# Kernel optimization log

Hardware: AMD Instinct MI355X
Metric: run time of the kernel (lower is better)

Reference implementation:

```python
import jax, jax.numpy as jnp
from jax import lax
import numpy as np

AXIS = 16      # axis_neuron
N_TYPES = 2    # number of atom types


def _mlp(x, Ws, bs):
    for W, b in zip(Ws, bs):
        x = jnp.tanh(x @ W + b)
    return x


def _forward(sym, dx, dy, dz, types,
             fw0, fb0, fw1, fb1, fw2, fb2,
             gw0, gb0, gw1, gb1, gw2, gb2, gwo, gbo):
    # sym/dx/dy/dz: (B, N, SEL, 4); types: (B, N) int
    N, SEL = sym.shape[1], sym.shape[2]

    def frame_fn(R, DX, DY, DZ, ty):
        E_atoms = jnp.zeros((N,), R.dtype)
        F = jnp.zeros((N, 3), R.dtype)
        for t in range(N_TYPES):  # loop over small fixed set of atom types
            mask = (ty == t).astype(R.dtype)            # (N,)
            cnt = jnp.maximum(mask.sum(), 1.0)
            m3 = mask[:, None, None]
            sji = R[:, :, 0:1]
            xyz = R[:, :, 1:4]
            ns = cnt * SEL
            nx = ns * 3.0
            s_avg = (sji * m3).sum() / ns
            x_avg = (xyz * m3).sum() / nx
            s_avg2 = ((sji ** 2) * m3).sum() / ns
            x_avg2 = ((xyz ** 2) * m3).sum() / nx
            avg2 = jnp.stack([s_avg2, x_avg2, x_avg2, x_avg2])
            avg1 = jnp.stack([s_avg, x_avg, x_avg, x_avg])
            std = jnp.sqrt(jnp.maximum(avg2 - avg1 ** 2, 0.0)) + 1e-8
            avg = jnp.stack([s_avg, 0.0 * s_avg, 0.0 * s_avg, 0.0 * s_avg])
            avg = lax.stop_gradient(avg)   # torch computes stats under no_grad
            std = lax.stop_gradient(std)
            Rn = (R - avg) / std
            DXn = DX / std
            DYn = DY / std
            DZn = DZ / std

            def etot(Rn_):
                s = Rn_[:, :, 0:1]                                  # (N, SEL, 1)
                G = _mlp(s, [fw0[t], fw1[t], fw2[t]], [fb0[t], fb1[t], fb2[t]])  # (N, SEL, M)
                RG = jnp.einsum('nsf,nsm->nfm', Rn_, G)             # (N, 4, M)
                GRRG = jnp.einsum('nfm,nfa->nma', RG, RG[:, :, :AXIS]).reshape(N, -1)  # (N, M*AXIS)
                denom = cnt * GRRG.shape[1]
                mu = (GRRG * mask[:, None]).sum() / denom
                mu2 = ((GRRG ** 2) * mask[:, None]).sum() / denom
                sd = jnp.sqrt(jnp.maximum(mu2 - mu ** 2, 0.0)) + 1e-8
                h = _mlp((GRRG - mu) / sd,
                         [gw0[t], gw1[t], gw2[t]], [gb0[t], gb1[t], gb2[t]])
                e = (h @ gwo[t] + gbo[t])[:, 0]                     # (N,)
                return (e * mask).sum(), e

            (Et, e_atoms), dR = jax.value_and_grad(etot, has_aux=True)(Rn)
            E_atoms = E_atoms + e_atoms * mask
            Fx = (dR * DXn).sum(axis=(1, 2))
            Fy = (dR * DYn).sum(axis=(1, 2))
            Fz = (dR * DZn).sum(axis=(1, 2))
            # "DO NOT forget to multiply -1 for F!!!"
            F = F - jnp.stack([Fx, Fy, Fz], axis=1) * mask[:, None]
        return E_atoms.sum(), F

    return jax.vmap(frame_fn)(sym, dx, dy, dz, types)


def setup_inputs() -> dict:
    key = jax.random.key(0)
    ks = jax.random.split(key, 24)
    B, N, SEL = 4, 1024, 128
    M = 100                     # filter_neuron[-1]
    FIT_IN = AXIS * M           # 1600
    d = {}
    d['sym'] = jax.random.normal(ks[0], (B, N, SEL, 4), jnp.float32)
    d['dx'] = jax.random.normal(ks[1], (B, N, SEL, 4), jnp.float32)
    d['dy'] = jax.random.normal(ks[2], (B, N, SEL, 4), jnp.float32)
    d['dz'] = jax.random.normal(ks[3], (B, N, SEL, 4), jnp.float32)
    d['types'] = jax.random.randint(ks[4], (B, N), 0, N_TYPES, jnp.int32)

    def w(k, shape):
        return jax.random.normal(k, shape, jnp.float32) / np.float32(np.sqrt(shape[-2]))

    def b(k, shape):
        return 0.1 * jax.random.normal(k, shape, jnp.float32)

    d['fw0'] = w(ks[5], (N_TYPES, 1, 25));      d['fb0'] = b(ks[6], (N_TYPES, 25))
    d['fw1'] = w(ks[7], (N_TYPES, 25, 50));     d['fb1'] = b(ks[8], (N_TYPES, 50))
    d['fw2'] = w(ks[9], (N_TYPES, 50, M));      d['fb2'] = b(ks[10], (N_TYPES, M))
    d['gw0'] = w(ks[11], (N_TYPES, FIT_IN, 240)); d['gb0'] = b(ks[12], (N_TYPES, 240))
    d['gw1'] = w(ks[13], (N_TYPES, 240, 240));  d['gb1'] = b(ks[14], (N_TYPES, 240))
    d['gw2'] = w(ks[15], (N_TYPES, 240, 240));  d['gb2'] = b(ks[16], (N_TYPES, 240))
    d['gwo'] = w(ks[17], (N_TYPES, 240, 1));    d['gbo'] = b(ks[18], (N_TYPES, 1))
    return d


def reference(sym, dx, dy, dz, types,
              fw0, fb0, fw1, fb1, fw2, fb2,
              gw0, gb0, gw1, gb1, gw2, gb2, gwo, gbo):
    return _forward(sym, dx, dy, dz, types,
                    fw0, fb0, fw1, fb1, fw2, fb2,
                    gw0, gb0, gw1, gb1, gw2, gb2, gwo, gbo)
```

## Files before the change

kernel.cpp:

```cpp
#include <hip/hip_runtime.h>

#define NBATCH 4
#define NATOM 1024
#define NSEL 128
#define H1 25
#define H2 50
#define HM 100
#define AX 16
#define GF 1600
#define FI 240
#define NT 2
#define NGRP64 18

#define WS_STATS_RAW 0
#define WS_STATS_FIN 64
#define WS_MUSD_RAW 128
#define WS_MUSD_FIN 144
#define WS_S_RAW 176
#define WS_CTR 192
#define WS_EBUF 256
#define WS_IDX (WS_EBUF + NBATCH*NATOM)
#define WS_G (WS_IDX + NBATCH*1152)
#define WS_P (WS_G + (size_t)NBATCH*NATOM*GF)
#define WS_BP0  (WS_P + (size_t)NBATCH*NATOM*GF)
#define WS_BP1  (WS_BP0 + (size_t)NT*15*50*256)
#define WS_BP2  (WS_BP1 + (size_t)NT*15*8*256)
#define WS_BPT2 (WS_BP2 + (size_t)NT*15*8*256)
#define WS_BPT1 (WS_BPT2 + (size_t)NT*15*8*256)
#define WS_BPT0 (WS_BPT1 + (size_t)NT*15*8*256)
#define WS_FW1T (WS_BPT0 + (size_t)NT*100*8*256)
#define WS_FW2T (WS_FW1T + (size_t)NT*H2*H1)
#define WS_RGB (WS_FW2T + (size_t)NT*HM*H2)
#define WS_GTB (WS_RGB + (size_t)NBATCH*NATOM*HM*4)
#define WS_GTB_UNITS ((size_t)NBATCH*NATOM*(HM/2)*NSEL)
#define WS_BF1B  (WS_GTB + WS_GTB_UNITS)
#define WS_BW2TB (WS_BF1B + (size_t)NT*1024)
#define WS_BW1TB (WS_BW2TB + (size_t)NT*4096)
#define WS_BF2B  (WS_BW1TB + (size_t)NT*1024)
#define WS_END   (WS_BF2B + (size_t)NT*3584)

#define GSTR 108

typedef __attribute__((ext_vector_type(8))) short bf16x8;
typedef __attribute__((ext_vector_type(4))) float f32x4;

__device__ __forceinline__ float ftanh(float x){
  float e = __expf(2.0f*x);
  return 1.0f - 2.0f/(e+1.0f);
}
__device__ __forceinline__ unsigned short f2bf(float x){
  unsigned b=__float_as_uint(x); b += 0x7FFF + ((b>>16)&1); return (unsigned short)(b>>16);
}
__device__ __forceinline__ float bf2f(unsigned short h){ return __uint_as_float(((unsigned)h)<<16); }
__device__ __forceinline__ float bflo(unsigned u){ return __uint_as_float(u<<16); }
__device__ __forceinline__ float bfhi(unsigned u){ return __uint_as_float(u & 0xFFFF0000u); }
__device__ __forceinline__ unsigned packbf(float a, float b){
  return (unsigned)f2bf(a) | ((unsigned)f2bf(b)<<16);
}

__device__ __forceinline__ float wave_sum(float v){
#pragma unroll
  for(int o=32;o>0;o>>=1) v += __shfl_down(v,o,64);
  return v;
}
__device__ __forceinline__ float block_sum2(float v, float* red){
  v = wave_sum(v);
  __syncthreads();
  if((threadIdx.x&63)==0) red[threadIdx.x>>6]=v;
  __syncthreads();
  return red[0]+red[1];
}
__device__ __forceinline__ float block_sum4(float v, float* red){
  v = wave_sum(v);
  __syncthreads();
  if((threadIdx.x&63)==0) red[threadIdx.x>>6]=v;
  __syncthreads();
  return red[0]+red[1]+red[2]+red[3];
}

__global__ void __launch_bounds__(256) k_transpose(const float* __restrict__ gw0,
    const float* __restrict__ gw1, const float* __restrict__ gw2,
    const float* __restrict__ fw1, const float* __restrict__ fw2, float* __restrict__ ws){
  const int cB0 = NT*15*50*256;
  const int cB1 = NT*15*8*256;
  const int cT0 = NT*100*8*256;
  const int c6 = NT*H2*H1, c7 = NT*HM*H2;
  const int total = cB0 + 4*cB1 + cT0 + c6 + c7;
  unsigned* wsu = (unsigned*)ws;
  for(int i = blockIdx.x*blockDim.x + threadIdx.x; i < total; i += gridDim.x*blockDim.x){
    if(i < cB0 + 4*cB1 + cT0){
      int base, NKs; const float* W; int KK; int mode; int t;
      int ii = i;
      if(ii < cB0){ base=WS_BP0; NKs=50; KK=1600; mode=0; t = ii/(15*50*256); ii -= t*(15*50*256); W = gw0 + (size_t)t*GF*FI; }
      else if(ii < cB0+cB1){ ii-=cB0; base=WS_BP1; NKs=8; KK=240; mode=0; t = ii/(15*8*256); ii -= t*(15*8*256); W = gw1 + t*FI*FI; }
      else if(ii < cB0+2*cB1){ ii-=cB0+cB1; base=WS_BP2; NKs=8; KK=240; mode=0; t = ii/(15*8*256); ii -= t*(15*8*256); W = gw2 + t*FI*FI; }
      else if(ii < cB0+3*cB1){ ii-=cB0+2*cB1; base=WS_BPT2; NKs=8; KK=240; mode=1; t = ii/(15*8*256); ii -= t*(15*8*256); W = gw2 + t*FI*FI; }
      else if(ii < cB0+4*cB1){ ii-=cB0+3*cB1; base=WS_BPT1; NKs=8; KK=240; mode=1; t = ii/(15*8*256); ii -= t*(15*8*256); W = gw1 + t*FI*FI; }
      else { ii-=cB0+4*cB1; base=WS_BPT0; NKs=8; KK=240; mode=2; t = ii/(100*8*256); ii -= t*(100*8*256); W = gw0 + (size_t)t*GF*FI; }
      int d = ii & 3;
      int lane = (ii>>2) & 63;
      int rem = ii >> 8;
      int ks = rem % NKs;
      int ntile = rem / NKs;
      int n = ntile*16 + (lane&15);
      int k0 = ks*32 + ((lane>>4)&3)*8 + 2*d;
      float v0, v1;
      if(mode==0){
        v0 = (k0   < KK) ? W[(size_t)(k0  )*FI + n] : 0.f;
        v1 = (k0+1 < KK) ? W[(size_t)(k0+1)*FI + n] : 0.f;
      } else if(mode==1){
        v0 = (k0   < KK) ? W[n*FI + k0  ] : 0.f;
        v1 = (k0+1 < KK) ? W[n*FI + k0+1] : 0.f;
      } else {
        v0 = (k0   < KK) ? W[(size_t)n*FI + k0  ] : 0.f;
        v1 = (k0+1 < KK) ? W[(size_t)n*FI + k0+1] : 0.f;
      }
      int telems = (base==WS_BP0) ? 15*50*256 : (base==WS_BPT0 ? 100*8*256 : 15*8*256);
      wsu[base + (size_t)t*telems + ii] = packbf(v0, v1);
    } else if(i < cB0 + 4*cB1 + cT0 + c6){
      int ii = i - (cB0+4*cB1+cT0); int t = ii/(H2*H1); int rem = ii - t*(H2*H1);
      int j = rem/H1; int k = rem - j*H1;
      ws[WS_FW1T + ii] = fw1[t*H1*H2 + k*H2 + j];
    } else {
      int ii = i - (cB0+4*cB1+cT0+c6); int t = ii/(HM*H2); int rem = ii - t*(HM*H2);
      int m = rem/H2; int j = rem - m*H2;
      ws[WS_FW2T + ii] = fw2[t*H2*HM + j*HM + m];
    }
  }
}

__global__ void __launch_bounds__(256) k_packf(const float* __restrict__ fw1,
    const float* __restrict__ fw2, float* __restrict__ ws){
  unsigned* wsu = (unsigned*)ws;
  const int c1 = NT*1024, c2 = NT*4096, c3 = NT*1024, c4 = NT*3584;
  const int total = c1 + c2 + c3 + c4;
  for(int i = blockIdx.x*blockDim.x + threadIdx.x; i < total; i += gridDim.x*blockDim.x){
    if(i < c1){
      int t = i/1024; int ii = i - t*1024;
      int nt = ii>>8; int lane = (ii>>2)&63; int d = ii&3;
      int n = nt*16 + (lane&15);
      int k0 = ((lane>>4)&3)*8 + 2*d;
      float v0 = (k0   < H1 && n < H2) ? fw1[t*H1*H2 + (k0  )*H2 + n] : 0.f;
      float v1 = (k0+1 < H1 && n < H2) ? fw1[t*H1*H2 + (k0+1)*H2 + n] : 0.f;
      wsu[WS_BF1B + i] = packbf(v0, v1);
    } else if(i < c1 + c2){
      int ii = i - c1; int t = ii/4096; ii -= t*4096;
      int nt = ii>>10; int ks = (ii>>8)&3; int lane = (ii>>2)&63; int d = ii&3;
      int n = nt*16 + (lane&15);
      int k0 = ks*32 + ((lane>>4)&3)*8 + 2*d;
      float v0 = (k0   < HM && n < H2) ? fw2[t*H2*HM + n*HM + k0  ] : 0.f;
      float v1 = (k0+1 < HM && n < H2) ? fw2[t*H2*HM + n*HM + k0+1] : 0.f;
      wsu[WS_BW2TB + ii + t*4096] = packbf(v0, v1);
    } else if(i < c1 + c2 + c3){
      int ii = i - c1 - c2; int t = ii/1024; ii -= t*1024;
      int nt = ii>>9; int ks = (ii>>8)&1; int lane = (ii>>2)&63; int d = ii&3;
      int n = nt*16 + (lane&15);
      int k0 = ks*32 + ((lane>>4)&3)*8 + 2*d;
      float v0 = (k0   < H2 && n < H1) ? fw1[t*H1*H2 + n*H2 + k0  ] : 0.f;
      float v1 = (k0+1 < H2 && n < H1) ? fw1[t*H1*H2 + n*H2 + k0+1] : 0.f;
      wsu[WS_BW1TB + ii + t*1024] = packbf(v0, v1);
    } else {
      int ii = i - c1 - c2 - c3; int t = ii/3584; ii -= t*3584;
      int nt = ii>>9; int ks = (ii>>8)&1; int lane = (ii>>2)&63; int d = ii&3;
      int n = nt*16 + (lane&15);
      int k0 = ks*32 + ((lane>>4)&3)*8 + 2*d;
      float v0 = (k0   < H2 && n < HM) ? fw2[t*H2*HM + (k0  )*HM + n] : 0.f;
      float v1 = (k0+1 < H2 && n < HM) ? fw2[t*H2*HM + (k0+1)*HM + n] : 0.f;
      wsu[WS_BF2B + ii + t*3584] = packbf(v0, v1);
    }
  }
}

__global__ void __launch_bounds__(256) k_stats(const float* __restrict__ sym,
    const int* __restrict__ types, float* __restrict__ ws){
  const int b = blockIdx.y;
  const int n0 = blockIdx.x * 64;
  const float* R = sym + ((size_t)b*NATOM + n0)*NSEL*4;
  const int* ty = types + b*NATOM;
  float ss0=0,ss20=0,xs0=0,xs20=0,ss1=0,ss21=0,xs1=0,xs21=0,c0=0,c1=0;
  for(int idx=threadIdx.x; idx<64*NSEL*4; idx+=256){
    int a = idx >> 9;
    int t = ty[n0+a];
    float v = R[idx];
    bool iss = (idx&3)==0;
    if(t==0){ if(iss){ss0+=v;ss20+=v*v;} else {xs0+=v;xs20+=v*v;} }
    else    { if(iss){ss1+=v;ss21+=v*v;} else {xs1+=v;xs21+=v*v;} }
  }
  if(threadIdx.x<64){ if(ty[n0+threadIdx.x]==0) c0=1.f; else c1=1.f; }
  ss0=wave_sum(ss0); ss20=wave_sum(ss20); xs0=wave_sum(xs0); xs20=wave_sum(xs20); c0=wave_sum(c0);
  ss1=wave_sum(ss1); ss21=wave_sum(ss21); xs1=wave_sum(xs1); xs21=wave_sum(xs21); c1=wave_sum(c1);
  if((threadIdx.x&63)==0){
    float* r0 = ws + WS_STATS_RAW + (b*2+0)*8;
    float* r1 = ws + WS_STATS_RAW + (b*2+1)*8;
    atomicAdd(r0+0,c0); atomicAdd(r0+1,ss0); atomicAdd(r0+2,ss20); atomicAdd(r0+3,xs0); atomicAdd(r0+4,xs20);
    atomicAdd(r1+0,c1); atomicAdd(r1+1,ss1); atomicAdd(r1+2,ss21); atomicAdd(r1+3,xs1); atomicAdd(r1+4,xs21);
  }
}

__global__ void k_fin_stats(float* ws){
  int i = threadIdx.x;
  if(i<8){
    float* raw = ws + WS_STATS_RAW + i*8;
    float cntf = fmaxf(raw[0], 1.f);
    float ns = cntf * (float)NSEL;
    float s_avg = raw[1]/ns, s_avg2 = raw[2]/ns;
    float x_avg = raw[3]/(ns*3.f), x_avg2 = raw[4]/(ns*3.f);
    float std_s = sqrtf(fmaxf(s_avg2 - s_avg*s_avg, 0.f)) + 1e-8f;
    float std_x = sqrtf(fmaxf(x_avg2 - x_avg*x_avg, 0.f)) + 1e-8f;
    float* fin = ws + WS_STATS_FIN + i*8;
    fin[0]=s_avg; fin[1]=1.f/std_s; fin[2]=1.f/std_x; fin[3]=cntf; fin[4]=raw[0];
  }
}

__global__ void k_index(const int* __restrict__ types, float* __restrict__ ws){
  int b = blockIdx.x;
  int rc0 = (int)ws[WS_STATS_FIN + (b*2)*8 + 4];
  int pad0 = (rc0+63)&~63;
  int* ctr = (int*)ws + WS_CTR;
  int* idx = (int*)ws + WS_IDX;
  for(int n=threadIdx.x;n<NATOM;n+=256){
    int t = types[b*NATOM+n];
    int pos = atomicAdd(&ctr[b*2+t],1);
    idx[b*1152 + (t ? pad0+pos : pos)] = n;
  }
}

__global__ void __launch_bounds__(128) k_fwdm(const float* __restrict__ sym, const int* __restrict__ types,
    const float* __restrict__ fw0,const float* __restrict__ fb0,
    const float* __restrict__ fb1,const float* __restrict__ fb2,
    float* __restrict__ ws){
  extern __shared__ char fraw[];
  float* Rn4 = (float*)fraw;
  float* RG4 = (float*)(fraw + 2048);
  float* red = (float*)(fraw + 3648);
  unsigned short* a2F = (unsigned short*)(fraw + 3680);
  unsigned* a2Fu = (unsigned*)(fraw + 3680);
  unsigned* a1L = (unsigned*)(fraw + 20576);
  unsigned short* Gl = (unsigned short*)(fraw + 20576);

  const int bid = blockIdx.x;
  const int b = bid >> 10;
  int t = types[bid];
  t = __builtin_amdgcn_readfirstlane(t);
  const float* fin = ws + WS_STATS_FIN + (b*2+t)*8;
  const float avg_s = fin[0], inv_ss = fin[1], inv_sx = fin[2];
  const int s = threadIdx.x;
  const int wave = s>>6, lane = s&63, lw = lane&15, lg = lane>>4;

  const float* W0 = fw0 + t*H1; const float* B0 = fb0 + t*H1;
  const float* B1 = fb1 + t*H2; const float* B2 = fb2 + t*HM;
  const unsigned* wsu = (const unsigned*)ws;
  const bf16x8* BF1 = (const bf16x8*)(wsu + WS_BF1B) + t*4*64;
  const bf16x8* BF2 = (const bf16x8*)(wsu + WS_BF2B) + t*14*64;

  float4 R4 = *(const float4*)&sym[(size_t)bid*NSEL*4 + s*4];
  float rn0 = (R4.x-avg_s)*inv_ss, rn1 = R4.y*inv_sx, rn2 = R4.z*inv_sx, rn3 = R4.w*inv_sx;
  *(float4*)&Rn4[s*4] = make_float4(rn0,rn1,rn2,rn3);

  {
    float a1r[H1];
#pragma unroll
    for(int kk=0;kk<H1;kk++) a1r[kk] = ftanh(rn0*W0[kk] + B0[kk]);
    unsigned* rw = a1L + s*17;
#pragma unroll
    for(int q=0;q<12;q++) rw[q] = packbf(a1r[2*q], a1r[2*q+1]);
    rw[12] = packbf(a1r[24], 0.f);
    rw[13]=0; rw[14]=0; rw[15]=0; rw[16]=0;
  }
  __syncthreads();

  const f32x4 fz = {0.f,0.f,0.f,0.f};
  for(int nt=0;nt<4;nt++){
    f32x4 acc[4];
#pragma unroll
    for(int mt=0;mt<4;mt++){
      int MT = wave*4 + mt;
      bf16x8 af = *(const bf16x8*)&a1L[(MT*16+lw)*17 + lg*4];
      acc[mt] = __builtin_amdgcn_mfma_f32_16x16x32_bf16(af, BF1[nt*64+lane], fz, 0,0,0);
    }
    int col = nt*16 + lw;
    float bias = (col<H2) ? B1[col] : 0.f;
#pragma unroll
    for(int mt=0;mt<4;mt++)
#pragma unroll
      for(int r=0;r<4;r++){
        int rw = (wave*4+mt)*16 + lg*4 + r;
        float v = (col<H2) ? ftanh(acc[mt][r] + bias) : 0.f;
        a2F[rw*66 + col] = f2bf(v);
      }
  }
  __syncthreads();
  for(int nt=0;nt<7;nt++){
    f32x4 acc[4];
#pragma unroll
    for(int mt=0;mt<4;mt++) acc[mt] = fz;
    for(int ks=0;ks<2;ks++){
#pragma unroll
      for(int mt=0;mt<4;mt++){
        int MT = wave*4 + mt;
        bf16x8 af = *(const bf16x8*)&a2Fu[(MT*16+lw)*33 + ks*16 + lg*4];
        acc[mt] = __builtin_amdgcn_mfma_f32_16x16x32_bf16(af, BF2[(nt*2+ks)*64+lane], acc[mt], 0,0,0);
      }
    }
    int col = nt*16 + lw;
    if(col < HM){
      float bias = B2[col];
#pragma unroll
      for(int mt=0;mt<4;mt++)
#pragma unroll
        for(int r=0;r<4;r++){
          int rw = (wave*4+mt)*16 + lg*4 + r;
          Gl[rw*GSTR + col] = f2bf(ftanh(acc[mt][r] + bias));
        }
    }
  }
  __syncthreads();
  if(s < HM){
    const int m = s;
    float a0=0,b0=0,c0=0,d0=0;
    for(int sn=0;sn<NSEL;sn++){
      float4 rn = *(const float4*)&Rn4[sn*4];
      float g = bf2f(Gl[sn*GSTR+m]);
      a0 += rn.x*g; b0 += rn.y*g; c0 += rn.z*g; d0 += rn.w*g;
    }
    *(float4*)&RG4[m*4] = make_float4(a0,b0,c0,d0);
  }
  __syncthreads();
  for(int i=s;i<HM*4;i+=128) ws[WS_RGB + (size_t)bid*(HM*4) + i] = RG4[i];
  {
    unsigned* GT = (unsigned*)ws + WS_GTB + (size_t)bid*((HM/2)*NSEL);
    for(int i=s;i<(HM/2)*NSEL;i+=128){
      int mp = i >> 7, ss = i & 127;
      GT[i] = *(const unsigned*)&Gl[ss*GSTR + 2*mp];
    }
  }
  float lsum=0,lsum2=0;
  float* gout = ws + WS_G + (size_t)bid*GF;
  for(int i=s;i<GF;i+=128){
    int m=i>>4, a=i&15;
    float4 rm = *(const float4*)&RG4[m*4];
    float4 ra = *(const float4*)&RG4[a*4];
    float gv = rm.x*ra.x + rm.y*ra.y + rm.z*ra.z + rm.w*ra.w;
    gout[i]=gv; lsum+=gv; lsum2+=gv*gv;
  }
  lsum = block_sum2(lsum, red);
  lsum2 = block_sum2(lsum2, red);
  if(s==0){
    atomicAdd(&ws[WS_MUSD_RAW + (b*2+t)*2 + 0], lsum);
    atomicAdd(&ws[WS_MUSD_RAW + (b*2+t)*2 + 1], lsum2);
  }
}

__global__ void __launch_bounds__(128) k_fwd(const float* __restrict__ sym, const int* __restrict__ types,
    const float* __restrict__ fw0,const float* __restrict__ fb0,
    const float* __restrict__ fb1,const float* __restrict__ fb2,
    float* __restrict__ ws){
  __shared__ float Rn4[NSEL*4];
  __shared__ unsigned short Gl[NSEL*GSTR];
  __shared__ float RG4[HM*4];
  __shared__ float red[8];

  const int bid = blockIdx.x;
  const int b = bid >> 10;
  int t = types[bid];
  t = __builtin_amdgcn_readfirstlane(t);
  const float* fin = ws + WS_STATS_FIN + (b*2+t)*8;
  const float avg_s = fin[0], inv_ss = fin[1], inv_sx = fin[2];
  const int s = threadIdx.x;

  const float* W0 = fw0 + t*H1; const float* B0 = fb0 + t*H1;
  const float* B1 = fb1 + t*H2; const float* B2 = fb2 + t*HM;
  const float* W1T = ws + WS_FW1T + t*H2*H1;
  const float* W2T = ws + WS_FW2T + t*HM*H2;

  float4 R4 = *(const float4*)&sym[(size_t)bid*NSEL*4 + s*4];
  float rn0 = (R4.x-avg_s)*inv_ss, rn1 = R4.y*inv_sx, rn2 = R4.z*inv_sx, rn3 = R4.w*inv_sx;
  *(float4*)&Rn4[s*4] = make_float4(rn0,rn1,rn2,rn3);

  float a1[H1];
#pragma unroll
  for(int k=0;k<H1;k++) a1[k] = ftanh(rn0*W0[k] + B0[k]);
  float a2[H2];
#pragma unroll
  for(int j=0;j<H2;j++){
    float acc = B1[j];
    const float* wr = W1T + j*H1;
#pragma unroll
    for(int k=0;k<H1;k++) acc += a1[k]*wr[k];
    a2[j] = ftanh(acc);
  }
  for(int m=0;m<HM;m+=4){
    const float* wr0 = W2T + m*H2; const float* wr1 = wr0 + H2;
    const float* wr2 = wr1 + H2;  const float* wr3 = wr2 + H2;
    float acc0 = B2[m], acc1 = B2[m+1], acc2 = B2[m+2], acc3 = B2[m+3];
#pragma unroll
    for(int j=0;j<H2;j++){
      float aj = a2[j];
      acc0 += aj*wr0[j]; acc1 += aj*wr1[j]; acc2 += aj*wr2[j]; acc3 += aj*wr3[j];
    }
    unsigned u0 = (unsigned)f2bf(ftanh(acc0)) | ((unsigned)f2bf(ftanh(acc1))<<16);
    unsigned u1 = (unsigned)f2bf(ftanh(acc2)) | ((unsigned)f2bf(ftanh(acc3))<<16);
    *(unsigned*)&Gl[s*GSTR + m] = u0;
    *(unsigned*)&Gl[s*GSTR + m + 2] = u1;
  }
  __syncthreads();
  if(s < HM){
    const int m = s;
    float a0=0,b0=0,c0=0,d0=0;
    for(int sn=0;sn<NSEL;sn++){
      float4 rn = *(const float4*)&Rn4[sn*4];
      float g = bf2f(Gl[sn*GSTR+m]);
      a0 += rn.x*g; b0 += rn.y*g; c0 += rn.z*g; d0 += rn.w*g;
    }
    *(float4*)&RG4[m*4] = make_float4(a0,b0,c0,d0);
  }
  __syncthreads();
  for(int i=s;i<HM*4;i+=128) ws[WS_RGB + (size_t)bid*(HM*4) + i] = RG4[i];
  float lsum=0,lsum2=0;
  float* gout = ws + WS_G + (size_t)bid*GF;
  for(int i=s;i<GF;i+=128){
    int m=i>>4, a=i&15;
    float4 rm = *(const float4*)&RG4[m*4];
    float4 ra = *(const float4*)&RG4[a*4];
    float gv = rm.x*ra.x + rm.y*ra.y + rm.z*ra.z + rm.w*ra.w;
    gout[i]=gv; lsum+=gv; lsum2+=gv*gv;
  }
  lsum = block_sum2(lsum, red);
  lsum2 = block_sum2(lsum2, red);
  if(s==0){
    atomicAdd(&ws[WS_MUSD_RAW + (b*2+t)*2 + 0], lsum);
    atomicAdd(&ws[WS_MUSD_RAW + (b*2+t)*2 + 1], lsum2);
  }
}

__global__ void k_fin_musd(float* ws){
  int i=threadIdx.x;
  if(i<8){
    float cntf = ws[WS_STATS_FIN + i*8 + 3];
    float denom = cntf * (float)GF;
    float Sg = ws[WS_MUSD_RAW + i*2], Sg2 = ws[WS_MUSD_RAW + i*2+1];
    float mu = Sg/denom, mu2 = Sg2/denom;
    float var = fmaxf(mu2 - mu*mu, 0.f);
    float r = sqrtf(var); float sd = r + 1e-8f;
    float* mf = ws + WS_MUSD_FIN + i*4;
    mf[0]=mu; mf[1]=1.f/sd; mf[2]=r; mf[3]=sd;
  }
}

__global__ void __launch_bounds__(256) k_fitm(
    const float* __restrict__ gb0,const float* __restrict__ gb1,
    const float* __restrict__ gb2,
    const float* __restrict__ gwo,const float* __restrict__ gbo,
    float* __restrict__ ws){
  extern __shared__ unsigned short lb[];
  unsigned short* h1S = lb;
  unsigned short* h2S = lb + 16896;
  unsigned short* dzA = lb + 33792;
  __shared__ float red[4];

  const int b = blockIdx.x / NGRP64;
  const int grp = blockIdx.x - b*NGRP64;
  int rc0 = (int)ws[WS_STATS_FIN + (b*2)*8 + 4];
  int rc1 = (int)ws[WS_STATS_FIN + (b*2+1)*8 + 4];
  rc0 = __builtin_amdgcn_readfirstlane(rc0);
  rc1 = __builtin_amdgcn_readfirstlane(rc1);
  const int pad0 = (rc0+63)&~63;
  const int tend = pad0 + ((rc1+63)&~63);
  const int slot0 = grp*64;
  if(slot0 >= tend) return;
  const int t = (slot0 >= pad0) ? 1 : 0;

  const float* mf = ws + WS_MUSD_FIN + (b*2+t)*4;
  const float mu = mf[0], isd = mf[1];

  const int tid = threadIdx.x;
  const int wave = tid>>6, lane = tid&63;
  const int lw = lane&15, lg = lane>>4;
  const int mRowBase = wave*16 + lg*4;

  const int* idx = (const int*)ws + WS_IDX + b*1152;
  int arow = idx[slot0 + wave*16 + lw];
  int rowSafe = arow<0?0:arow;
  const float* yrowA = ws + WS_G + (size_t)(b*NATOM + rowSafe)*GF;
  int idC[4];
#pragma unroll
  for(int r=0;r<4;r++) idC[r] = idx[slot0 + wave*16 + lg*4 + r];

  const unsigned* wsu = (const unsigned*)ws;
  const bf16x8* BP0  = (const bf16x8*)(wsu + WS_BP0)  + (size_t)t*15*50*64;
  const bf16x8* BP1  = (const bf16x8*)(wsu + WS_BP1)  + t*15*8*64;
  const bf16x8* BP2  = (const bf16x8*)(wsu + WS_BP2)  + t*15*8*64;
  const bf16x8* BPT2 = (const bf16x8*)(wsu + WS_BPT2) + t*15*8*64;
  const bf16x8* BPT1 = (const bf16x8*)(wsu + WS_BPT1) + t*15*8*64;
  const bf16x8* BPT0 = (const bf16x8*)(wsu + WS_BPT0) + (size_t)t*100*8*64;

  for(int i=tid;i<64*24;i+=256){
    int r = i/24, c = 240 + (i - (i/24)*24);
    h1S[r*264+c]=0; h2S[r*264+c]=0; dzA[r*264+c]=0;
  }

  f32x4 acc[15];
  const f32x4 fz = {0.f,0.f,0.f,0.f};
#pragma unroll
  for(int nt=0;nt<15;nt++) acc[nt] = fz;
  for(int ks=0;ks<50;ks++){
    float4 y0 = *(const float4*)(yrowA + ks*32 + lg*8);
    float4 y1 = *(const float4*)(yrowA + ks*32 + lg*8 + 4);
    union{ unsigned u[4]; bf16x8 v; } A;
    A.u[0]=packbf((y0.x-mu)*isd,(y0.y-mu)*isd); A.u[1]=packbf((y0.z-mu)*isd,(y0.w-mu)*isd);
    A.u[2]=packbf((y1.x-mu)*isd,(y1.y-mu)*isd); A.u[3]=packbf((y1.z-mu)*isd,(y1.w-mu)*isd);
#pragma unroll
    for(int nt=0;nt<15;nt++)
      acc[nt] = __builtin_amdgcn_mfma_f32_16x16x32_bf16(A.v, BP0[(nt*50+ks)*64+lane], acc[nt], 0,0,0);
  }
#pragma unroll
  for(int nt=0;nt<15;nt++){
    float bias = gb0[t*FI + nt*16 + lw];
#pragma unroll
    for(int r=0;r<4;r++){
      float h = ftanh(acc[nt][r] + bias);
      h1S[(mRowBase+r)*264 + nt*16 + lw] = f2bf(h);
    }
  }
  __syncthreads();
#pragma unroll
  for(int nt=0;nt<15;nt++) acc[nt] = fz;
  for(int ks=0;ks<8;ks++){
    bf16x8 a = *(const bf16x8*)&h1S[(wave*16+lw)*264 + ks*32 + lg*8];
#pragma unroll
    for(int nt=0;nt<15;nt++)
      acc[nt] = __builtin_amdgcn_mfma_f32_16x16x32_bf16(a, BP1[(nt*8+ks)*64+lane], acc[nt], 0,0,0);
  }
#pragma unroll
  for(int nt=0;nt<15;nt++){
    float bias = gb1[t*FI + nt*16 + lw];
#pragma unroll
    for(int r=0;r<4;r++){
      float h = ftanh(acc[nt][r] + bias);
      h2S[(mRowBase+r)*264 + nt*16 + lw] = f2bf(h);
    }
  }
  __syncthreads();
#pragma unroll
  for(int nt=0;nt<15;nt++) acc[nt] = fz;
  for(int ks=0;ks<8;ks++){
    bf16x8 a = *(const bf16x8*)&h2S[(wave*16+lw)*264 + ks*32 + lg*8];
#pragma unroll
    for(int nt=0;nt<15;nt++)
      acc[nt] = __builtin_amdgcn_mfma_f32_16x16x32_bf16(a, BP2[(nt*8+ks)*64+lane], acc[nt], 0,0,0);
  }
  float pe[4] = {0.f,0.f,0.f,0.f};
#pragma unroll
  for(int nt=0;nt<15;nt++){
    float bias = gb2[t*FI + nt*16 + lw];
    float wo = gwo[t*FI + nt*16 + lw];
#pragma unroll
    for(int r=0;r<4;r++){
      float h = ftanh(acc[nt][r] + bias);
      pe[r] += h*wo;
      float d3 = wo*(1.f - h*h);
      dzA[(mRowBase+r)*264 + nt*16 + lw] = f2bf(d3);
    }
  }
#pragma unroll
  for(int o=1;o<16;o<<=1){
#pragma unroll
    for(int r=0;r<4;r++) pe[r] += __shfl_xor(pe[r], o, 64);
  }
  if(lw==0){
#pragma unroll
    for(int r=0;r<4;r++) if(idC[r]>=0) ws[WS_EBUF + b*NATOM + idC[r]] = pe[r] + gbo[t];
  }
  __syncthreads();
#pragma unroll
  for(int nt=0;nt<15;nt++) acc[nt] = fz;
  for(int ks=0;ks<8;ks++){
    bf16x8 a = *(const bf16x8*)&dzA[(wave*16+lw)*264 + ks*32 + lg*8];
#pragma unroll
    for(int nt=0;nt<15;nt++)
      acc[nt] = __builtin_amdgcn_mfma_f32_16x16x32_bf16(a, BPT2[(nt*8+ks)*64+lane], acc[nt], 0,0,0);
  }
#pragma unroll
  for(int nt=0;nt<15;nt++){
#pragma unroll
    for(int r=0;r<4;r++){
      float h2 = bf2f(h2S[(mRowBase+r)*264 + nt*16 + lw]);
      acc[nt][r] *= (1.f - h2*h2);
    }
  }
  __syncthreads();
#pragma unroll
  for(int nt=0;nt<15;nt++){
#pragma unroll
    for(int r=0;r<4;r++) dzA[(mRowBase+r)*264 + nt*16 + lw] = f2bf(acc[nt][r]);
  }
  __syncthreads();
#pragma unroll
  for(int nt=0;nt<15;nt++) acc[nt] = fz;
  for(int ks=0;ks<8;ks++){
    bf16x8 a = *(const bf16x8*)&dzA[(wave*16+lw)*264 + ks*32 + lg*8];
#pragma unroll
    for(int nt=0;nt<15;nt++)
      acc[nt] = __builtin_amdgcn_mfma_f32_16x16x32_bf16(a, BPT1[(nt*8+ks)*64+lane], acc[nt], 0,0,0);
  }
#pragma unroll
  for(int nt=0;nt<15;nt++){
#pragma unroll
    for(int r=0;r<4;r++){
      float h1 = bf2f(h1S[(mRowBase+r)*264 + nt*16 + lw]);
      acc[nt][r] *= (1.f - h1*h1);
    }
  }
  __syncthreads();
#pragma unroll
  for(int nt=0;nt<15;nt++){
#pragma unroll
    for(int r=0;r<4;r++) dzA[(mRowBase+r)*264 + nt*16 + lw] = f2bf(acc[nt][r]);
  }
  __syncthreads();
  const float* yG = ws + WS_G + (size_t)b*NATOM*GF;
  float* pP = ws + WS_P + (size_t)b*NATOM*GF;
  float s1t=0.f, syt=0.f;
  for(int c0=0;c0<100;c0+=10){
    f32x4 pc[10];
#pragma unroll
    for(int j=0;j<10;j++) pc[j] = fz;
    for(int ks=0;ks<8;ks++){
      bf16x8 a = *(const bf16x8*)&dzA[(wave*16+lw)*264 + ks*32 + lg*8];
#pragma unroll
      for(int j=0;j<10;j++)
        pc[j] = __builtin_amdgcn_mfma_f32_16x16x32_bf16(a, BPT0[((c0+j)*8+ks)*64+lane], pc[j], 0,0,0);
    }
#pragma unroll
    for(int j=0;j<10;j++){
      int n = (c0+j)*16 + lw;
#pragma unroll
      for(int r=0;r<4;r++){
        if(idC[r]>=0){
          float pv = pc[j][r];
          size_t off = (size_t)idC[r]*GF + n;
          pP[off] = pv;
          s1t += pv;
          syt += pv * (yG[off]-mu)*isd;
        }
      }
    }
  }
  s1t = block_sum4(s1t, red);
  syt = block_sum4(syt, red);
  if(tid==0){
    atomicAdd(&ws[WS_S_RAW+(b*2+t)*2+0], s1t);
    atomicAdd(&ws[WS_S_RAW+(b*2+t)*2+1], syt);
  }
}

__global__ void __launch_bounds__(128) k_bwdm2(const float* __restrict__ sym,
    const float* __restrict__ dxp,const float* __restrict__ dyp,const float* __restrict__ dzp,
    const int* __restrict__ types,
    const float* __restrict__ fw0,const float* __restrict__ fb0,
    const float* __restrict__ fb1,
    float* __restrict__ ws, float* __restrict__ out){
  extern __shared__ char lraw[];
  float* dRG4 = (float*)lraw;
  float* red  = (float*)(lraw + 1600);
  float* dgb  = (float*)(lraw + 1664);
  float* RG4  = (float*)(lraw + 8464);
  unsigned short* a2L = (unsigned short*)(lraw + 1664);
  unsigned* dz2u = (unsigned*)(lraw + 14720);
  unsigned short* dz2s = (unsigned short*)(lraw + 14720);
  unsigned* ML = (unsigned*)(lraw + 27648);
  unsigned short* dz1L = (unsigned short*)(lraw + 27648);

  const int bid = blockIdx.x;
  const int b = bid >> 10;
  int t = types[bid];
  t = __builtin_amdgcn_readfirstlane(t);
  const float* fin = ws + WS_STATS_FIN + (b*2+t)*8;
  const float avg_s=fin[0], inv_ss=fin[1], inv_sx=fin[2], cntf=fin[3];
  const float* mf = ws + WS_MUSD_FIN + (b*2+t)*4;
  const float mu=mf[0], inv_sd=mf[1], rr=mf[2];
  const float S1 = ws[WS_S_RAW + (b*2+t)*2 + 0];
  const float Sy = ws[WS_S_RAW + (b*2+t)*2 + 1];
  const float denom = cntf * (float)GF;
  const float c1 = S1/denom;
  const float c2 = (rr>0.f) ? (Sy/denom)/rr : 0.f;
  const int s = threadIdx.x;
  const int wave = s>>6, lane = s&63, lw = lane&15, lg = lane>>4;

  const float* W0 = fw0 + t*H1; const float* B0 = fb0 + t*H1;
  const float* B1f = fb1 + t*H2;
  const unsigned* wsu = (const unsigned*)ws;
  const bf16x8* BF1  = (const bf16x8*)(wsu + WS_BF1B)  + t*4*64;
  const bf16x8* BW2T = (const bf16x8*)(wsu + WS_BW2TB) + t*16*64;
  const bf16x8* BW1T = (const bf16x8*)(wsu + WS_BW1TB) + t*4*64;

  if(s < 32) ((unsigned*)(lraw + 14720))[128*25 + s] = 0;
  if(s < 64) ML[128*51 + s] = 0;

  for(int i=s;i<HM*4;i+=128) RG4[i] = ws[WS_RGB + (size_t)bid*(HM*4) + i];
  __syncthreads();
  const float* p = ws + WS_P + (size_t)bid*GF;
  for(int i=s;i<GF;i+=128){
    int m=i>>4, a=i&15;
    float4 rm = *(const float4*)&RG4[m*4];
    float4 ra = *(const float4*)&RG4[a*4];
    float gv = rm.x*ra.x + rm.y*ra.y + rm.z*ra.z + rm.w*ra.w;
    float yv = (gv-mu)*inv_sd;
    dgb[m*17+a] = (p[i]-c1)*inv_sd - yv*c2;
  }
  __syncthreads();
  if(s < HM){
    const int m = s;
    float a0=0,b0=0,c0=0,d0=0;
#pragma unroll
    for(int a=0;a<AX;a++){
      float d = dgb[m*17+a];
      float4 r = *(const float4*)&RG4[a*4];
      a0 += d*r.x; b0 += d*r.y; c0 += d*r.z; d0 += d*r.w;
    }
    if(m<AX){
      for(int mp=0;mp<HM;mp++){
        float d = dgb[mp*17+m];
        float4 r = *(const float4*)&RG4[mp*4];
        a0 += d*r.x; b0 += d*r.y; c0 += d*r.z; d0 += d*r.w;
      }
    }
    *(float4*)&dRG4[m*4] = make_float4(a0,b0,c0,d0);
  }
  float4 R4 = *(const float4*)&sym[(size_t)bid*NSEL*4 + s*4];
  float rn0 = (R4.x-avg_s)*inv_ss, rn1 = R4.y*inv_sx, rn2 = R4.z*inv_sx, rn3 = R4.w*inv_sx;
  {
    float a1r[H1];
#pragma unroll
    for(int kk=0;kk<H1;kk++) a1r[kk] = ftanh(rn0*W0[kk] + B0[kk]);
    unsigned* row = ML + s*51;
#pragma unroll
    for(int q=0;q<12;q++) row[q] = packbf(a1r[2*q], a1r[2*q+1]);
    row[12] = packbf(a1r[24], 0.f);
    row[13]=0; row[14]=0; row[15]=0; row[16]=0;
  }
  __syncthreads();

  const f32x4 fz = {0.f,0.f,0.f,0.f};
  for(int nt=0;nt<4;nt++){
    f32x4 acc[4];
#pragma unroll
    for(int mt=0;mt<4;mt++){
      bf16x8 af = *(const bf16x8*)&ML[((wave*4+mt)*16+lw)*51 + lg*4];
      acc[mt] = __builtin_amdgcn_mfma_f32_16x16x32_bf16(af, BF1[nt*64+lane], fz, 0,0,0);
    }
    int col = nt*16 + lw;
    if(col < H2){
      float bias = B1f[col];
#pragma unroll
      for(int mt=0;mt<4;mt++)
#pragma unroll
        for(int r=0;r<4;r++){
          int rw = (wave*4+mt)*16 + lg*4 + r;
          a2L[rw*51 + col] = f2bf(ftanh(acc[mt][r] + bias));
        }
    }
  }
  __syncthreads();
  const unsigned* GT = (const unsigned*)ws + WS_GTB + (size_t)bid*((HM/2)*NSEL);
  float drn0=0,drn1=0,drn2=0,drn3=0;
  {
    unsigned* row = ML + s*51;
    for(int q=0;q<50;q++){
      int m0 = 2*q;
      unsigned u = GT[q*NSEL + s];
      float g0 = bflo(u), g1 = bfhi(u);
      float4 dm0 = *(const float4*)&dRG4[m0*4];
      float4 dm1 = *(const float4*)&dRG4[(m0+1)*4];
      drn0 += dm0.x*g0 + dm1.x*g1;
      drn1 += dm0.y*g0 + dm1.y*g1;
      drn2 += dm0.z*g0 + dm1.z*g1;
      drn3 += dm0.w*g0 + dm1.w*g1;
      float d30 = (dm0.x*rn0 + dm0.y*rn1 + dm0.z*rn2 + dm0.w*rn3)*(1.f-g0*g0);
      float d31 = (dm1.x*rn0 + dm1.y*rn1 + dm1.z*rn2 + dm1.w*rn3)*(1.f-g1*g1);
      row[q] = packbf(d30, d31);
    }
    row[50] = 0;
  }
  __syncthreads();
  for(int nt=0;nt<4;nt++){
    f32x4 acc[4];
#pragma unroll
    for(int mt=0;mt<4;mt++) acc[mt] = fz;
    for(int ks=0;ks<4;ks++){
#pragma unroll
      for(int mt=0;mt<4;mt++){
        bf16x8 af = *(const bf16x8*)&ML[((wave*4+mt)*16+lw)*51 + ks*16 + lg*4];
        acc[mt] = __builtin_amdgcn_mfma_f32_16x16x32_bf16(af, BW2T[(nt*4+ks)*64+lane], acc[mt], 0,0,0);
      }
    }
    int col = nt*16 + lw;
    if(col < H2){
#pragma unroll
      for(int mt=0;mt<4;mt++)
#pragma unroll
        for(int r=0;r<4;r++){
          int rw = (wave*4+mt)*16 + lg*4 + r;
          float a2v = bf2f(a2L[rw*51 + col]);
          dz2s[rw*50 + col] = f2bf(acc[mt][r]*(1.f - a2v*a2v));
        }
    }
  }
  __syncthreads();
  for(int nt2=0;nt2<2;nt2++){
    f32x4 acc[4];
#pragma unroll
    for(int mt=0;mt<4;mt++) acc[mt] = fz;
    for(int ks2=0;ks2<2;ks2++){
#pragma unroll
      for(int mt=0;mt<4;mt++){
        bf16x8 af = *(const bf16x8*)&dz2u[((wave*4+mt)*16+lw)*25 + ks2*16 + lg*4];
        acc[mt] = __builtin_amdgcn_mfma_f32_16x16x32_bf16(af, BW1T[(nt2*2+ks2)*64+lane], acc[mt], 0,0,0);
      }
    }
    int col = nt2*16 + lw;
    if(col < 28){
#pragma unroll
      for(int mt=0;mt<4;mt++)
#pragma unroll
        for(int r=0;r<4;r++){
          int rw = (wave*4+mt)*16 + lg*4 + r;
          dz1L[rw*28 + col] = f2bf((col<H1) ? acc[mt][r] : 0.f);
        }
    }
  }
  __syncthreads();
  {
    float ds = 0.f;
#pragma unroll
    for(int kk=0;kk<H1;kk++){
      float w0v = W0[kk];
      float a1v = ftanh(rn0*w0v + B0[kk]);
      float d1 = bf2f(dz1L[s*28 + kk]);
      ds += d1*(1.f - a1v*a1v)*w0v;
    }
    drn0 += ds;
  }
  float w0 = drn0*inv_ss, w1 = drn1*inv_sx, w2 = drn2*inv_sx, w3 = drn3*inv_sx;
  float4 X = *(const float4*)&dxp[(size_t)bid*NSEL*4 + s*4];
  float4 Y = *(const float4*)&dyp[(size_t)bid*NSEL*4 + s*4];
  float4 Z = *(const float4*)&dzp[(size_t)bid*NSEL*4 + s*4];
  float fx = w0*X.x + w1*X.y + w2*X.z + w3*X.w;
  float fy = w0*Y.x + w1*Y.y + w2*Y.z + w3*Y.w;
  float fz2 = w0*Z.x + w1*Z.y + w2*Z.z + w3*Z.w;
  fx = wave_sum(fx); fy = wave_sum(fy); fz2 = wave_sum(fz2);
  __syncthreads();
  if((s&63)==0){ int w=s>>6; red[w*3+0]=fx; red[w*3+1]=fy; red[w*3+2]=fz2; }
  __syncthreads();
  if(s==0){
    float* F = out + 4 + (size_t)bid*3;
    F[0] = -(red[0]+red[3]);
    F[1] = -(red[1]+red[4]);
    F[2] = -(red[2]+red[5]);
  }
}

__global__ void __launch_bounds__(128) k_bwd0(const float* __restrict__ sym,
    const float* __restrict__ dxp,const float* __restrict__ dyp,const float* __restrict__ dzp,
    const int* __restrict__ types,
    const float* __restrict__ fw0,const float* __restrict__ fb0,
    const float* __restrict__ fw1,const float* __restrict__ fb1,
    const float* __restrict__ fb2,
    float* __restrict__ ws, float* __restrict__ out){
  __shared__ float RG4[HM*4];
  __shared__ float dgb[HM*17];
  __shared__ float dRG4[HM*4];
  __shared__ float red[8];

  const int bid = blockIdx.x;
  const int b = bid >> 10;
  int t = types[bid];
  t = __builtin_amdgcn_readfirstlane(t);
  const float* fin = ws + WS_STATS_FIN + (b*2+t)*8;
  const float avg_s=fin[0], inv_ss=fin[1], inv_sx=fin[2], cntf=fin[3];
  const float* mf = ws + WS_MUSD_FIN + (b*2+t)*4;
  const float mu=mf[0], inv_sd=mf[1], rr=mf[2];
  const float S1 = ws[WS_S_RAW + (b*2+t)*2 + 0];
  const float Sy = ws[WS_S_RAW + (b*2+t)*2 + 1];
  const float denom = cntf * (float)GF;
  const float c1 = S1/denom;
  const float c2 = (rr>0.f) ? (Sy/denom)/rr : 0.f;
  const int s = threadIdx.x;

  const float* W0 = fw0 + t*H1; const float* B0 = fb0 + t*H1;
  const float* B1 = fb1 + t*H2; const float* B2 = fb2 + t*HM;
  const float* W1  = fw1 + t*H1*H2;
  const float* W1T = ws + WS_FW1T + t*H2*H1;
  const float* W2T = ws + WS_FW2T + t*HM*H2;

  for(int i=s;i<HM*4;i+=128) RG4[i] = ws[WS_RGB + (size_t)bid*(HM*4) + i];
  __syncthreads();

  const float* p = ws + WS_P + (size_t)bid*GF;
  for(int i=s;i<GF;i+=128){
    int m=i>>4, a=i&15;
    float4 rm = *(const float4*)&RG4[m*4];
    float4 ra = *(const float4*)&RG4[a*4];
    float gv = rm.x*ra.x + rm.y*ra.y + rm.z*ra.z + rm.w*ra.w;
    float yv = (gv-mu)*inv_sd;
    dgb[m*17+a] = (p[i]-c1)*inv_sd - yv*c2;
  }
  __syncthreads();
  if(s < HM){
    const int m = s;
    float a0=0,b0=0,c0=0,d0=0;
#pragma unroll
    for(int a=0;a<AX;a++){
      float d = dgb[m*17+a];
      float4 r = *(const float4*)&RG4[a*4];
      a0 += d*r.x; b0 += d*r.y; c0 += d*r.z; d0 += d*r.w;
    }
    if(m<AX){
      for(int mp=0;mp<HM;mp++){
        float d = dgb[mp*17+m];
        float4 r = *(const float4*)&RG4[mp*4];
        a0 += d*r.x; b0 += d*r.y; c0 += d*r.z; d0 += d*r.w;
      }
    }
    *(float4*)&dRG4[m*4] = make_float4(a0,b0,c0,d0);
  }
  __syncthreads();

  float4 R4 = *(const float4*)&sym[(size_t)bid*NSEL*4 + s*4];
  float rn0 = (R4.x-avg_s)*inv_ss, rn1 = R4.y*inv_sx, rn2 = R4.z*inv_sx, rn3 = R4.w*inv_sx;

  float a1[H1];
#pragma unroll
  for(int kk=0;kk<H1;kk++) a1[kk] = ftanh(rn0*W0[kk] + B0[kk]);
  float a2[H2];
#pragma unroll
  for(int j=0;j<H2;j++){
    float acc = B1[j];
    const float* wr = W1T + j*H1;
#pragma unroll
    for(int kk=0;kk<H1;kk++) acc += a1[kk]*wr[kk];
    a2[j] = ftanh(acc);
  }

  float dz2a[H2];
#pragma unroll
  for(int j=0;j<H2;j++) dz2a[j]=0.f;
  float drn0=0,drn1=0,drn2=0,drn3=0;
  for(int m=0;m<HM;m+=4){
    const float* wr0 = W2T + m*H2; const float* wr1 = wr0 + H2;
    const float* wr2 = wr1 + H2;  const float* wr3 = wr2 + H2;
    float acc0 = B2[m], acc1 = B2[m+1], acc2 = B2[m+2], acc3 = B2[m+3];
#pragma unroll
    for(int j=0;j<H2;j++){
      float aj = a2[j];
      acc0 += aj*wr0[j]; acc1 += aj*wr1[j]; acc2 += aj*wr2[j]; acc3 += aj*wr3[j];
    }
    float g0 = ftanh(acc0), g1 = ftanh(acc1), g2 = ftanh(acc2), g3 = ftanh(acc3);
    float4 d0 = *(const float4*)&dRG4[m*4];
    float4 d1 = *(const float4*)&dRG4[(m+1)*4];
    float4 d2 = *(const float4*)&dRG4[(m+2)*4];
    float4 d3 = *(const float4*)&dRG4[(m+3)*4];
    drn0 += d0.x*g0 + d1.x*g1 + d2.x*g2 + d3.x*g3;
    drn1 += d0.y*g0 + d1.y*g1 + d2.y*g2 + d3.y*g3;
    drn2 += d0.z*g0 + d1.z*g1 + d2.z*g2 + d3.z*g3;
    drn3 += d0.w*g0 + d1.w*g1 + d2.w*g2 + d3.w*g3;
    float dz30 = (d0.x*rn0 + d0.y*rn1 + d0.z*rn2 + d0.w*rn3)*(1.f-g0*g0);
    float dz31 = (d1.x*rn0 + d1.y*rn1 + d1.z*rn2 + d1.w*rn3)*(1.f-g1*g1);
    float dz32 = (d2.x*rn0 + d2.y*rn1 + d2.z*rn2 + d2.w*rn3)*(1.f-g2*g2);
    float dz33 = (d3.x*rn0 + d3.y*rn1 + d3.z*rn2 + d3.w*rn3)*(1.f-g3*g3);
#pragma unroll
    for(int j=0;j<H2;j++) dz2a[j] += dz30*wr0[j] + dz31*wr1[j] + dz32*wr2[j] + dz33*wr3[j];
  }
#pragma unroll
  for(int j=0;j<H2;j++){ float av=a2[j]; dz2a[j] *= (1.f-av*av); }
  float dsacc=0.f;
#pragma unroll
  for(int kk=0;kk<H1;kk++){
    const float* wr = W1 + kk*H2;
    float acc=0.f;
#pragma unroll
    for(int j=0;j<H2;j++) acc += dz2a[j]*wr[j];
    float av=a1[kk];
    dsacc += acc*(1.f-av*av)*W0[kk];
  }
  drn0 += dsacc;
  float w0 = drn0*inv_ss, w1 = drn1*inv_sx, w2 = drn2*inv_sx, w3 = drn3*inv_sx;
  float4 X = *(const float4*)&dxp[(size_t)bid*NSEL*4 + s*4];
  float4 Y = *(const float4*)&dyp[(size_t)bid*NSEL*4 + s*4];
  float4 Z = *(const float4*)&dzp[(size_t)bid*NSEL*4 + s*4];
  float fx = w0*X.x + w1*X.y + w2*X.z + w3*X.w;
  float fy = w0*Y.x + w1*Y.y + w2*Y.z + w3*Y.w;
  float fz = w0*Z.x + w1*Z.y + w2*Z.z + w3*Z.w;
  fx = wave_sum(fx); fy = wave_sum(fy); fz = wave_sum(fz);
  __syncthreads();
  if((s&63)==0){ int w=s>>6; red[w*3+0]=fx; red[w*3+1]=fy; red[w*3+2]=fz; }
  __syncthreads();
  if(s==0){
    float* F = out + 4 + (size_t)bid*3;
    F[0] = -(red[0]+red[3]);
    F[1] = -(red[1]+red[4]);
    F[2] = -(red[2]+red[5]);
  }
}

__global__ void k_write_E(const float* __restrict__ ws, float* __restrict__ out){
  __shared__ float red[8];
  const int b = blockIdx.x;
  const float* e = ws + WS_EBUF + b*NATOM;
  float sv=0;
  for(int i=threadIdx.x;i<NATOM;i+=256) sv+=e[i];
  sv = block_sum4(sv, red);
  if(threadIdx.x==0) out[b]=sv;
}

extern "C" void kernel_launch(void* const* d_in, const int* in_sizes, int n_in,
                              void* d_out, int out_size, void* d_ws, size_t ws_size,
                              hipStream_t stream) {
  const float* sym = (const float*)d_in[0];
  const float* dxp = (const float*)d_in[1];
  const float* dyp = (const float*)d_in[2];
  const float* dzp = (const float*)d_in[3];
  const int*   types=(const int*)d_in[4];
  const float* fw0=(const float*)d_in[5];
  const float* fb0=(const float*)d_in[6];
  const float* fw1=(const float*)d_in[7];
  const float* fb1=(const float*)d_in[8];
  const float* fw2=(const float*)d_in[9];
  const float* fb2=(const float*)d_in[10];
  const float* gw0=(const float*)d_in[11];
  const float* gb0=(const float*)d_in[12];
  const float* gw1=(const float*)d_in[13];
  const float* gb1=(const float*)d_in[14];
  const float* gw2=(const float*)d_in[15];
  const float* gb2=(const float*)d_in[16];
  const float* gwo=(const float*)d_in[17];
  const float* gbo=(const float*)d_in[18];
  float* ws = (float*)d_ws;
  float* out = (float*)d_out;

  const size_t need_bytes = (size_t)WS_END * 4;
  const int storeGT = (ws_size >= need_bytes) ? 1 : 0;

  hipMemsetAsync(d_ws, 0, 1024, stream);
  hipMemsetAsync((char*)d_ws + (size_t)WS_IDX*4, 0xFF, (size_t)NBATCH*1152*4, stream);

  k_transpose<<<1024,256,0,stream>>>(gw0,gw1,gw2,fw1,fw2,ws);
  if(storeGT) k_packf<<<64,256,0,stream>>>(fw1,fw2,ws);
  k_stats<<<dim3(16,NBATCH),256,0,stream>>>(sym,types,ws);
  k_fin_stats<<<1,64,0,stream>>>(ws);
  k_index<<<NBATCH,256,0,stream>>>(types,ws);

  if(storeGT){
    const int lds_fwdm = 48224;
    hipFuncSetAttribute((const void*)k_fwdm, hipFuncAttributeMaxDynamicSharedMemorySize, lds_fwdm);
    k_fwdm<<<NBATCH*NATOM,128,lds_fwdm,stream>>>(sym,types,fw0,fb0,fb1,fb2,ws);
  } else {
    k_fwd<<<NBATCH*NATOM,128,0,stream>>>(sym,types,fw0,fb0,fb1,fb2,ws);
  }
  k_fin_musd<<<1,64,0,stream>>>(ws);

  const int lds_fitm = 3*64*264*2;
  hipFuncSetAttribute((const void*)k_fitm, hipFuncAttributeMaxDynamicSharedMemorySize, lds_fitm);
  k_fitm<<<NBATCH*NGRP64,256,lds_fitm,stream>>>(gb0,gb1,gb2,gwo,gbo,ws);

  if(storeGT){
    const int lds_bwdm = 54016;
    hipFuncSetAttribute((const void*)k_bwdm2, hipFuncAttributeMaxDynamicSharedMemorySize, lds_bwdm);
    k_bwdm2<<<NBATCH*NATOM,128,lds_bwdm,stream>>>(sym,dxp,dyp,dzp,types,fw0,fb0,fb1,ws,out);
  } else {
    k_bwd0<<<NBATCH*NATOM,128,0,stream>>>(sym,dxp,dyp,dzp,types,fw0,fb0,fw1,fb1,fb2,ws,out);
  }

  k_write_E<<<NBATCH,256,0,stream>>>(ws,out);
}
```

Before: 856.3 us.

## Split fitting-net input-gradient GEMM into separate chunked kernel for more parallelism

Moves the final dz·W0ᵀ projection (100 column tiles writing the 1600-wide P gradient) out of k_fitm into a new k_pm kernel. k_fitm now writes its bf16 dz tile to a workspace buffer, and k_pm runs five blocks per group, each handling 20 of the 100 column tiles. This spreads the heaviest output-writing stage over five times as many workgroups (72 blocks → 360), making better use of CUs. The cost is an extra launch plus a global store and reload of the dz tile.

```diff
diff --git a/kernel.cpp b/kernel.cpp
--- a/kernel.cpp
+++ b/kernel.cpp
@@ -11,6 +11,7 @@
 #define FI 240
 #define NT 2
 #define NGRP64 18
+#define PCH 5
 
 #define WS_STATS_RAW 0
 #define WS_STATS_FIN 64
@@ -37,7 +38,8 @@
 #define WS_BW2TB (WS_BF1B + (size_t)NT*1024)
 #define WS_BW1TB (WS_BW2TB + (size_t)NT*4096)
 #define WS_BF2B  (WS_BW1TB + (size_t)NT*1024)
-#define WS_END   (WS_BF2B + (size_t)NT*3584)
+#define WS_DZ1  (WS_BF2B + (size_t)NT*3584)
+#define WS_END  (WS_DZ1 + (size_t)NBATCH*NGRP64*8448)
 
 #define GSTR 108
 
@@ -456,7 +458,6 @@
   unsigned short* h1S = lb;
   unsigned short* h2S = lb + 16896;
   unsigned short* dzA = lb + 33792;
-  __shared__ float red[4];
 
   const int b = blockIdx.x / NGRP64;
   const int grp = blockIdx.x - b*NGRP64;
@@ -492,7 +493,6 @@
   const bf16x8* BP2  = (const bf16x8*)(wsu + WS_BP2)  + t*15*8*64;
   const bf16x8* BPT2 = (const bf16x8*)(wsu + WS_BPT2) + t*15*8*64;
   const bf16x8* BPT1 = (const bf16x8*)(wsu + WS_BPT1) + t*15*8*64;
-  const bf16x8* BPT0 = (const bf16x8*)(wsu + WS_BPT0) + (size_t)t*100*8*64;
 
   for(int i=tid;i<64*24;i+=256){
     int r = i/24, c = 240 + (i - (i/24)*24);
@@ -618,10 +618,58 @@
     for(int r=0;r<4;r++) dzA[(mRowBase+r)*264 + nt*16 + lw] = f2bf(acc[nt][r]);
   }
   __syncthreads();
+  {
+    unsigned* dzOut = (unsigned*)ws + WS_DZ1 + (size_t)blockIdx.x*8448;
+    const unsigned* dzAu = (const unsigned*)dzA;
+    for(int i=tid;i<8448;i+=256) dzOut[i] = dzAu[i];
+  }
+}
+
+__global__ void __launch_bounds__(256) k_pm(float* __restrict__ ws){
+  extern __shared__ unsigned short lb[];
+  unsigned short* dzA = lb;
+  __shared__ float red[4];
+
+  const int gid = blockIdx.x / PCH;
+  const int chunk = blockIdx.x - gid*PCH;
+  const int b = gid / NGRP64;
+  const int grp = gid - b*NGRP64;
+  int rc0 = (int)ws[WS_STATS_FIN + (b*2)*8 + 4];
+  int rc1 = (int)ws[WS_STATS_FIN + (b*2+1)*8 + 4];
+  rc0 = __builtin_amdgcn_readfirstlane(rc0);
+  rc1 = __builtin_amdgcn_readfirstlane(rc1);
+  const int pad0 = (rc0+63)&~63;
+  const int tend = pad0 + ((rc1+63)&~63);
+  const int slot0 = grp*64;
+  if(slot0 >= tend) return;
+  const int t = (slot0 >= pad0) ? 1 : 0;
+
+  const float* mf = ws + WS_MUSD_FIN + (b*2+t)*4;
+  const float mu = mf[0], isd = mf[1];
+  const int tid = threadIdx.x;
+  const int wave = tid>>6, lane = tid&63, lw = lane&15, lg = lane>>4;
+
+  const int* idx = (const int*)ws + WS_IDX + b*1152;
+  int idC[4];
+#pragma unroll
+  for(int r=0;r<4;r++) idC[r] = idx[slot0 + wave*16 + lg*4 + r];
+
+  const unsigned* wsu = (const unsigned*)ws;
+  const bf16x8* BPT0 = (const bf16x8*)(wsu + WS_BPT0) + (size_t)t*100*8*64;
+
+  {
+    const unsigned* src = (const unsigned*)ws + WS_DZ1 + (size_t)gid*8448;
+    unsigned* dst = (unsigned*)lb;
+    for(int i=tid;i<8448;i+=256) dst[i] = src[i];
+  }
+  __syncthreads();
+
+  const f32x4 fz = {0.f,0.f,0.f,0.f};
   const float* yG = ws + WS_G + (size_t)b*NATOM*GF;
   float* pP = ws + WS_P + (size_t)b*NATOM*GF;
   float s1t=0.f, syt=0.f;
-  for(int c0=0;c0<100;c0+=10){
+  for(int sc=0;sc<2;sc++){
+    int c0 = chunk*20 + sc*10;
     f32x4 pc[10];
 #pragma unroll
     for(int j=0;j<10;j++) pc[j] = fz;
@@ -1063,6 +1111,10 @@
   hipFuncSetAttribute((const void*)k_fitm, hipFuncAttributeMaxDynamicSharedMemorySize, lds_fitm);
   k_fitm<<<NBATCH*NGRP64,256,lds_fitm,stream>>>(gb0,gb1,gb2,gwo,gbo,ws);
 
+  const int lds_pm = 64*264*2;
+  hipFuncSetAttribute((const void*)k_pm, hipFuncAttributeMaxDynamicSharedMemorySize, lds_pm);
+  k_pm<<<NBATCH*NGRP64*PCH,256,lds_pm,stream>>>(ws);
+
   if(storeGT){
     const int lds_bwdm = 54016;
     hipFuncSetAttribute((const void*)k_bwdm2, hipFuncAttributeMaxDynamicSharedMemorySize, lds_bwdm);
```

Measured after the change: 777.7 us. -9.2%, faster.
